# Optimization experiments

Hardware: AMD Instinct MI355X
Metric: run time of the kernel (lower is better)

## Reference

```python
import jax, jax.numpy as jnp
import numpy as np

T, B, I, H = 512, 64, 1024, 1024


def setup_inputs() -> dict:
    key = jax.random.key(0)
    k1, k2, k3, k4, k5, k6 = jax.random.split(key, 6)
    bound = 1.0 / np.sqrt(H)  # torch RNNCell init: U(-1/sqrt(H), 1/sqrt(H))
    return {
        "input": jax.random.normal(k1, (T, B, I), dtype=jnp.float32),
        "hidden": jax.random.normal(k2, (B, H), dtype=jnp.float32),
        "W_ih": jax.random.uniform(k3, (H, I), minval=-bound, maxval=bound, dtype=jnp.float32),
        "W_hh": jax.random.uniform(k4, (H, H), minval=-bound, maxval=bound, dtype=jnp.float32),
        "b_ih": jax.random.uniform(k5, (H,), minval=-bound, maxval=bound, dtype=jnp.float32),
        "b_hh": jax.random.uniform(k6, (H,), minval=-bound, maxval=bound, dtype=jnp.float32),
    }


def reference(input, hidden, W_ih, W_hh, b_ih, b_hh):
    # Precompute input projections for all timesteps in one big GEMM:
    # [T,B,I] @ [I,H] -> [T,B,H]
    x_proj = jnp.einsum("tbi,hi->tbh", input, W_ih) + b_ih + b_hh

    def step(h, xp):
        # h' = tanh(x W_ih^T + b_ih + h W_hh^T + b_hh)
        h_new = jnp.tanh(xp + h @ W_hh.T)
        return h_new, h_new

    h_last, output = jax.lax.scan(step, hidden, x_proj)
    return output, h_last
```

## Files before the change

### kernel.cpp

```cpp
#include <hip/hip_runtime.h>
#include <hip/hip_bf16.h>
#include <math.h>

#define T_STEPS 512
#define BATCH   64
#define IN_DIM  1024
#define HID     1024
#define BH_SZ   (BATCH * HID)

typedef short bf16x8 __attribute__((ext_vector_type(8)));
typedef float f32x4  __attribute__((ext_vector_type(4)));
typedef unsigned u32x4 __attribute__((ext_vector_type(4)));
typedef unsigned long long u64;

__device__ __forceinline__ unsigned ld_coh_u32(const unsigned* p) {
    return __hip_atomic_load(p, __ATOMIC_RELAXED, __HIP_MEMORY_SCOPE_AGENT);
}
__device__ __forceinline__ void st_coh_u32(unsigned* p, unsigned v) {
    __hip_atomic_store(p, v, __ATOMIC_RELAXED, __HIP_MEMORY_SCOPE_AGENT);
}
__device__ __forceinline__ u64 ld_coh_u64(const u64* p) {
    return __hip_atomic_load(p, __ATOMIC_RELAXED, __HIP_MEMORY_SCOPE_AGENT);
}

__device__ __forceinline__ unsigned short f2bf(float x) {
    unsigned u = __builtin_bit_cast(unsigned, x);
    unsigned r = u + 0x7FFFu + ((u >> 16) & 1u);
    return (unsigned short)(r >> 16);
}
__device__ __forceinline__ float bf2f(unsigned short h) {
    unsigned u = ((unsigned)h) << 16;
    return __builtin_bit_cast(float, u);
}
__device__ __forceinline__ float fast_tanh(float x) {
    float e = __expf(2.0f * x);
    return 1.0f - 2.0f * __builtin_amdgcn_rcpf(e + 1.0f);
}

__global__ __launch_bounds__(256) void pack_x_kernel(
    const float* __restrict__ src, unsigned short* __restrict__ dst, int n8)
{
    int idx = blockIdx.x * 256 + threadIdx.x;
    int stride = gridDim.x * 256;
    for (int i = idx; i < n8; i += stride) {
        float4 a = *(const float4*)(src + (size_t)i * 8);
        float4 b = *(const float4*)(src + (size_t)i * 8 + 4);
        float vv[8] = {a.x, a.y, a.z, a.w, b.x, b.y, b.z, b.w};
        bf16x8 o;
        #pragma unroll
        for (int e = 0; e < 8; e++) o[e] = (short)f2bf(vv[e]);
        *(bf16x8*)(dst + (size_t)i * 8) = o;
    }
}

__global__ __launch_bounds__(512, 1) void rnn_fused_kernel(
    const float* __restrict__ x,
    const unsigned short* __restrict__ xp16,
    const float* __restrict__ h0,
    const float* __restrict__ W_ih,
    const float* __restrict__ Whh,
    const float* __restrict__ b_ih,
    const float* __restrict__ b_hh,
    float* __restrict__ out,
    unsigned* hcomm,
    unsigned* flags)
{
    __shared__ unsigned short Wih[16 * 1024];
    __shared__ unsigned short Hhi[16 * 1024];
    __shared__ unsigned short Hlo[16 * 1024];
    __shared__ unsigned short Xh [16 * 1024];
    __shared__ f32x4 Pred[8][64];

    const int bid = blockIdx.x;
    const int j0 = (bid & 63) * 16;
    const int b0 = (bid >> 6) * 16;
    const int tid  = threadIdx.x;
    const int lane = tid & 63;
    const int w    = tid >> 6;

    const int frow = lane & 15;
    const int ksub = (lane >> 4) * 8;
    const int sw   = (frow & 7) << 3;

    #pragma unroll
    for (int i = 0; i < 4; i++) {
        int c = i * 512 + tid;
        int row = c >> 7;
        int k0 = (c & 127) * 8;
        const float* src = W_ih + (size_t)(j0 + row) * IN_DIM + k0;
        float4 v0 = *(const float4*)(src);
        float4 v1 = *(const float4*)(src + 4);
        float vv[8] = {v0.x, v0.y, v0.z, v0.w, v1.x, v1.y, v1.z, v1.w};
        bf16x8 hi8;
        #pragma unroll
        for (int e = 0; e < 8; e++) hi8[e] = (short)f2bf(vv[e]);
        int ofs = row * 1024 + (k0 ^ ((row & 7) << 3));
        *(bf16x8*)&Wih[ofs] = hi8;
    }

    #pragma unroll
    for (int i = 0; i < 4; i++) {
        int c = i * 512 + tid;
        int row = c >> 7;
        int k0 = (c & 127) * 8;
        const float* src = Whh + (size_t)(j0 + row) * HID + k0;
        float4 v0 = *(const float4*)(src);
        float4 v1 = *(const float4*)(src + 4);
        float vv[8] = {v0.x, v0.y, v0.z, v0.w, v1.x, v1.y, v1.z, v1.w};
        bf16x8 hi8, lo8;
        #pragma unroll
        for (int e = 0; e < 8; e++) {
            unsigned short h = f2bf(vv[e]);
            hi8[e] = (short)h;
            lo8[e] = (short)f2bf(vv[e] - bf2f(h));
        }
        int ofs = row * 1024 + (k0 ^ ((row & 7) << 3));
        *(bf16x8*)&Hhi[ofs] = hi8;
        *(bf16x8*)&Hlo[ofs] = lo8;
    }
    __syncthreads();
    bf16x8 wh[4], wl[4];
    #pragma unroll
    for (int kk = 0; kk < 4; kk++) {
        int kidx = w * 128 + kk * 32 + ksub;
        int ofs  = frow * 1024 + (kidx ^ sw);
        wh[kk] = *(const bf16x8*)&Hhi[ofs];
        wl[kk] = *(const bf16x8*)&Hlo[ofs];
    }
    __syncthreads();

    if (xp16) {
        #pragma unroll
        for (int i = 0; i < 4; i++) {
            int c = i * 512 + tid;
            int row = c >> 7;
            int k0 = (c & 127) * 8;
            bf16x8 hi8 = *(const bf16x8*)(xp16 + (size_t)(b0 + row) * IN_DIM + k0);
            int ofs = row * 1024 + (k0 ^ ((row & 7) << 3));
            *(bf16x8*)&Xh[ofs] = hi8;
        }
    } else {
        #pragma unroll
        for (int i = 0; i < 4; i++) {
            int c = i * 512 + tid;
            int row = c >> 7;
            int k0 = (c & 127) * 8;
            const float* p = x + (size_t)(b0 + row) * IN_DIM + k0;
            float4 v0 = *(const float4*)(p);
            float4 v1 = *(const float4*)(p + 4);
            float vv[8] = {v0.x, v0.y, v0.z, v0.w, v1.x, v1.y, v1.z, v1.w};
            bf16x8 hi8;
            #pragma unroll
            for (int e = 0; e < 8; e++) hi8[e] = (short)f2bf(vv[e]);
            int ofs = row * 1024 + (k0 ^ ((row & 7) << 3));
            *(bf16x8*)&Xh[ofs] = hi8;
        }
    }

    const int o = tid;
    const size_t out_off = (size_t)(b0 + (o >> 4)) * HID + (size_t)(j0 + (o & 15));
    float bias = 0.f;
    if (tid < 256) bias = b_ih[j0 + (o & 15)] + b_hh[j0 + (o & 15)];

    for (int t = 0; t < T_STEPS; t++) {
        if (t == 0) {
            #pragma unroll
            for (int i = 0; i < 4; i++) {
                int c = i * 512 + tid;
                int row = c >> 7;
                int k0 = (c & 127) * 8;
                const float* p = h0 + (size_t)(b0 + row) * HID + k0;
                float4 v0 = *(const float4*)(p);
                float4 v1 = *(const float4*)(p + 4);
                float vv[8] = {v0.x, v0.y, v0.z, v0.w, v1.x, v1.y, v1.z, v1.w};
                bf16x8 hi8, lo8;
                #pragma unroll
                for (int e = 0; e < 8; e++) {
                    unsigned short h = f2bf(vv[e]);
                    hi8[e] = (short)h;
                    lo8[e] = (short)f2bf(vv[e] - bf2f(h));
                }
                int ofs = row * 1024 + (k0 ^ ((row & 7) << 3));
                *(bf16x8*)&Hhi[ofs] = hi8;
                *(bf16x8*)&Hlo[ofs] = lo8;
            }
        } else {
            const u64* hsrc64 = (const u64*)(hcomm + (size_t)((t + 1) & 1) * BH_SZ);
            u64 pv[16];
            #pragma unroll
            for (int i = 0; i < 4; i++) {
                int c = i * 512 + tid;
                int row = c >> 7;
                int k0 = (c & 127) * 8;
                const u64* p = hsrc64 + (((size_t)(b0 + row) * HID + k0) >> 1);
                #pragma unroll
                for (int e = 0; e < 4; e++)
                    pv[i * 4 + e] = ld_coh_u64(p + e);
            }
            #pragma unroll
            for (int i = 0; i < 4; i++) {
                int c = i * 512 + tid;
                int row = c >> 7;
                int k0 = (c & 127) * 8;
                u32x4 hiu, lou;
                #pragma unroll
                for (int e = 0; e < 4; e++) {
                    u64 q = pv[i * 4 + e];
                    unsigned p0 = (unsigned)q;
                    unsigned p1 = (unsigned)(q >> 32);
                    hiu[e] = (p0 & 0xFFFFu) | (p1 << 16);
                    lou[e] = (p0 >> 16) | (p1 & 0xFFFF0000u);
                }
                int ofs = row * 1024 + (k0 ^ ((row & 7) << 3));
                *(u32x4*)&Hhi[ofs] = hiu;
                *(u32x4*)&Hlo[ofs] = lou;
            }
        }
        __syncthreads();

        {
            f32x4 acc0 = {0.f, 0.f, 0.f, 0.f};
            f32x4 acc1 = {0.f, 0.f, 0.f, 0.f};
            #pragma unroll
            for (int kk = 0; kk < 4; kk++) {
                int kidx = w * 128 + kk * 32 + ksub;
                int ofs  = frow * 1024 + (kidx ^ sw);
                bf16x8 ahi = *(const bf16x8*)&Hhi[ofs];
                bf16x8 alo = *(const bf16x8*)&Hlo[ofs];
                bf16x8 xh  = *(const bf16x8*)&Xh[ofs];
                bf16x8 wi  = *(const bf16x8*)&Wih[ofs];
                acc0 = __builtin_amdgcn_mfma_f32_16x16x32_bf16(ahi, wh[kk], acc0, 0, 0, 0);
                acc1 = __builtin_amdgcn_mfma_f32_16x16x32_bf16(ahi, wl[kk], acc1, 0, 0, 0);
                acc0 = __builtin_amdgcn_mfma_f32_16x16x32_bf16(alo, wh[kk], acc0, 0, 0, 0);
                acc1 = __builtin_amdgcn_mfma_f32_16x16x32_bf16(xh,  wi,     acc1, 0, 0, 0);
            }
            Pred[w][lane] = acc0 + acc1;
        }
        __syncthreads();

        float hn = 0.f;
        if (tid < 256) {
            const int b = o >> 4, j = o & 15;
            const int plane = ((b >> 2) << 4) | j;
            const int pr = b & 3;
            float s = bias;
            #pragma unroll
            for (int k = 0; k < 8; k++) s += Pred[k][plane][pr];
            hn = fast_tanh(s);
            unsigned short hi = f2bf(hn);
            unsigned short lo = f2bf(hn - bf2f(hi));
            unsigned pk = (unsigned)hi | ((unsigned)lo << 16);
            st_coh_u32(hcomm + (size_t)(t & 1) * BH_SZ + out_off, pk);
        }
        __syncthreads();

        if (tid == 0) st_coh_u32(&flags[bid * 32], (unsigned)(t + 1));

        if (tid < 256) {
            out[(size_t)t * BH_SZ + out_off] = hn;
            if (t == T_STEPS - 1)
                out[(size_t)T_STEPS * BH_SZ + out_off] = hn;
        }
        if (t + 1 < T_STEPS) {
            if (xp16) {
                const unsigned short* xs = xp16 + (size_t)(t + 1) * BH_SZ;
                #pragma unroll
                for (int i = 0; i < 4; i++) {
                    int c = i * 512 + tid;
                    int row = c >> 7;
                    int k0 = (c & 127) * 8;
                    bf16x8 hi8 = *(const bf16x8*)(xs + (size_t)(b0 + row) * IN_DIM + k0);
                    int ofs = row * 1024 + (k0 ^ ((row & 7) << 3));
                    *(bf16x8*)&Xh[ofs] = hi8;
                }
            } else {
                const float* xs = x + (size_t)(t + 1) * BH_SZ;
                #pragma unroll
                for (int i = 0; i < 4; i++) {
                    int c = i * 512 + tid;
                    int row = c >> 7;
                    int k0 = (c & 127) * 8;
                    const float* p = xs + (size_t)(b0 + row) * IN_DIM + k0;
                    float4 v0 = *(const float4*)(p);
                    float4 v1 = *(const float4*)(p + 4);
                    float vv[8] = {v0.x, v0.y, v0.z, v0.w, v1.x, v1.y, v1.z, v1.w};
                    bf16x8 hi8;
                    #pragma unroll
                    for (int e = 0; e < 8; e++) hi8[e] = (short)f2bf(vv[e]);
                    int ofs = row * 1024 + (k0 ^ ((row & 7) << 3));
                    *(bf16x8*)&Xh[ofs] = hi8;
                }
            }
        }

        if (tid < 64) {
            const unsigned target = (unsigned)(t + 1);
            for (;;) {
                int ok = 1;
                #pragma unroll
                for (int g = 0; g < 4; g++) {
                    unsigned v = ld_coh_u32(&flags[(size_t)(tid + g * 64) * 32]);
                    ok &= (v >= target) ? 1 : 0;
                }
                if (__all(ok)) break;
                __builtin_amdgcn_s_sleep(4);
            }
        }
        __syncthreads();
    }
}

extern "C" void kernel_launch(void* const* d_in, const int* in_sizes, int n_in,
                              void* d_out, int out_size, void* d_ws, size_t ws_size,
                              hipStream_t stream)
{
    const float* input  = (const float*)d_in[0];
    const float* hidden = (const float*)d_in[1];
    const float* W_ih   = (const float*)d_in[2];
    const float* W_hh   = (const float*)d_in[3];
    const float* b_ih   = (const float*)d_in[4];
    const float* b_hh   = (const float*)d_in[5];
    float* out = (float*)d_out;

    unsigned* flags = (unsigned*)d_ws;
    unsigned* hcomm = (unsigned*)((char*)d_ws + 256 * 32 * sizeof(unsigned));
    hipMemsetAsync(flags, 0, 256 * 32 * sizeof(unsigned), stream);

    const size_t xpk_off  = (size_t)1 << 20;
    const size_t xpk_size = (size_t)T_STEPS * BH_SZ * sizeof(unsigned short);
    const unsigned short* xp16 = nullptr;
    if (ws_size >= xpk_off + xpk_size) {
        unsigned short* xp = (unsigned short*)((char*)d_ws + xpk_off);
        pack_x_kernel<<<2048, 256, 0, stream>>>(input, xp,
                                                (T_STEPS * BATCH * IN_DIM) / 8);
        xp16 = xp;
    }

    rnn_fused_kernel<<<256, 512, 0, stream>>>(
        input, xp16, hidden, W_ih, W_hh, b_ih, b_hh, out, hcomm, flags);
}
```

Baseline: 2.311 ms.

## Move epilogue into one wavefront and overlap next-step X load with barrier wait

The per-step epilogue (bias, reduction over partial sums, tanh, hi/lo bf16 packing) now runs in a single wavefront. Each lane handles four outputs and writes them with 64-bit coherent stores and a float4 output store. That wave publishes the flag right after an s_waitcnt, without a block-wide __syncthreads. The other waves stage the next timestep's input tile into LDS while the first wave spins on the grid flags, so one barrier per step is removed and the X load overlaps the inter-block wait. In exchange, the tanh work is concentrated in fewer threads and the X staging is spread over 448 threads with a guarded tail.

New measurement: 2.881 ms. 24.7% more time.

```diff
diff --git a/kernel.cpp b/kernel.cpp
--- a/kernel.cpp
+++ b/kernel.cpp
@@ -22,6 +22,9 @@
 __device__ __forceinline__ u64 ld_coh_u64(const u64* p) {
     return __hip_atomic_load(p, __ATOMIC_RELAXED, __HIP_MEMORY_SCOPE_AGENT);
 }
+__device__ __forceinline__ void st_coh_u64(u64* p, u64 v) {
+    __hip_atomic_store(p, v, __ATOMIC_RELAXED, __HIP_MEMORY_SCOPE_AGENT);
+}
 
 __device__ __forceinline__ unsigned short f2bf(float x) {
     unsigned u = __builtin_bit_cast(unsigned, x);
@@ -35,6 +38,11 @@
 __device__ __forceinline__ float fast_tanh(float x) {
     float e = __expf(2.0f * x);
     return 1.0f - 2.0f * __builtin_amdgcn_rcpf(e + 1.0f);
+}
+__device__ __forceinline__ unsigned pack_hl(float v) {
+    unsigned short hi = f2bf(v);
+    unsigned short lo = f2bf(v - bf2f(hi));
+    return (unsigned)hi | ((unsigned)lo << 16);
 }
 
 __global__ __launch_bounds__(256) void pack_x_kernel(
@@ -157,10 +165,17 @@
         }
     }
 
-    const int o = tid;
-    const size_t out_off = (size_t)(b0 + (o >> 4)) * HID + (size_t)(j0 + (o & 15));
-    float bias = 0.f;
-    if (tid < 256) bias = b_ih[j0 + (o & 15)] + b_hh[j0 + (o & 15)];
+    const int bloc  = lane >> 2;
+    const int jb    = (4 * lane) & 15;
+    const int prr   = bloc & 3;
+    const int pbase = (bloc >> 2) << 4;
+    const size_t woff = (size_t)(b0 + bloc) * HID + j0 + jb;
+    float bias4[4];
+    if (tid < 64) {
+        #pragma unroll
+        for (int i = 0; i < 4; i++)
+            bias4[i] = b_ih[j0 + jb + i] + b_hh[j0 + jb + i];
+    }
 
     for (int t = 0; t < T_STEPS; t++) {
         if (t == 0) {
@@ -238,74 +253,76 @@
         }
         __syncthreads();
 
-        float hn = 0.f;
-        if (tid < 256) {
-            const int b = o >> 4, j = o & 15;
-            const int plane = ((b >> 2) << 4) | j;
-            const int pr = b & 3;
-            float s = bias;
-            #pragma unroll
-            for (int k = 0; k < 8; k++) s += Pred[k][plane][pr];
-            hn = fast_tanh(s);
-            unsigned short hi = f2bf(hn);
-            unsigned short lo = f2bf(hn - bf2f(hi));
-            unsigned pk = (unsigned)hi | ((unsigned)lo << 16);
-            st_coh_u32(hcomm + (size_t)(t & 1) * BH_SZ + out_off, pk);
-        }
-        __syncthreads();
-
-        if (tid == 0) st_coh_u32(&flags[bid * 32], (unsigned)(t + 1));
-
-        if (tid < 256) {
-            out[(size_t)t * BH_SZ + out_off] = hn;
+        if (tid < 64) {
+            float hn4[4];
+            #pragma unroll
+            for (int i = 0; i < 4; i++) {
+                float s = bias4[i];
+                const int plane = pbase | (jb + i);
+                #pragma unroll
+                for (int k = 0; k < 8; k++) s += Pred[k][plane][prr];
+                hn4[i] = fast_tanh(s);
+            }
+            u64* dst = (u64*)(hcomm + (size_t)(t & 1) * BH_SZ + woff);
+            u64 w0 = (u64)pack_hl(hn4[0]) | ((u64)pack_hl(hn4[1]) << 32);
+            u64 w1 = (u64)pack_hl(hn4[2]) | ((u64)pack_hl(hn4[3]) << 32);
+            st_coh_u64(dst, w0);
+            st_coh_u64(dst + 1, w1);
+            asm volatile("s_waitcnt vmcnt(0)" ::: "memory");
+            if (lane == 0) st_coh_u32(&flags[bid * 32], (unsigned)(t + 1));
+            float4 o4 = make_float4(hn4[0], hn4[1], hn4[2], hn4[3]);
+            *(float4*)(out + (size_t)t * BH_SZ + woff) = o4;
             if (t == T_STEPS - 1)
-                out[(size_t)T_STEPS * BH_SZ + out_off] = hn;
-        }
-        if (t + 1 < T_STEPS) {
-            if (xp16) {
-                const unsigned short* xs = xp16 + (size_t)(t + 1) * BH_SZ;
-                #pragma unroll
-                for (int i = 0; i < 4; i++) {
-                    int c = i * 512 + tid;
-                    int row = c >> 7;
-                    int k0 = (c & 127) * 8;
-                    bf16x8 hi8 = *(const bf16x8*)(xs + (size_t)(b0 + row) * IN_DIM + k0);
-                    int ofs = row * 1024 + (k0 ^ ((row & 7) << 3));
-                    *(bf16x8*)&Xh[ofs] = hi8;
-                }
-            } else {
-                const float* xs = x + (size_t)(t + 1) * BH_SZ;
-                #pragma unroll
-                for (int i = 0; i < 4; i++) {
-                    int c = i * 512 + tid;
-                    int row = c >> 7;
-                    int k0 = (c & 127) * 8;
-                    const float* p = xs + (size_t)(b0 + row) * IN_DIM + k0;
-                    float4 v0 = *(const float4*)(p);
-                    float4 v1 = *(const float4*)(p + 4);
-                    float vv[8] = {v0.x, v0.y, v0.z, v0.w, v1.x, v1.y, v1.z, v1.w};
-                    bf16x8 hi8;
-                    #pragma unroll
-                    for (int e = 0; e < 8; e++) hi8[e] = (short)f2bf(vv[e]);
-                    int ofs = row * 1024 + (k0 ^ ((row & 7) << 3));
-                    *(bf16x8*)&Xh[ofs] = hi8;
-                }
-            }
-        }
-
-        if (tid < 64) {
+                *(float4*)(out + (size_t)T_STEPS * BH_SZ + woff) = o4;
             const unsigned target = (unsigned)(t + 1);
             for (;;) {
                 int ok = 1;
                 #pragma unroll
                 for (int g = 0; g < 4; g++) {
-                    unsigned v = ld_coh_u32(&flags[(size_t)(tid + g * 64) * 32]);
+                    unsigned v = ld_coh_u32(&flags[(size_t)(lane + g * 64) * 32]);
                     ok &= (v >= target) ? 1 : 0;
                 }
                 if (__all(ok)) break;
                 __builtin_amdgcn_s_sleep(4);
             }
-        }
+        } else if (t + 1 < T_STEPS) {
+            const int tt = tid - 64;
+            if (xp16) {
+                const unsigned short* xs = xp16 + (size_t)(t + 1) * BH_SZ;
+                #pragma unroll
+                for (int i = 0; i < 5; i++) {
+                    int c = i * 448 + tt;
+                    if (c < 2048) {
+                        int row = c >> 7;
+                        int k0 = (c & 127) * 8;
+                        bf16x8 hi8 = *(const bf16x8*)(xs + (size_t)(b0 + row) * IN_DIM + k0);
+                        int ofs = row * 1024 + (k0 ^ ((row & 7) << 3));
+                        *(bf16x8*)&Xh[ofs] = hi8;
+                    }
+                }
+            } else {
+                const float* xs = x + (size_t)(t + 1) * BH_SZ;
+                #pragma unroll
+                for (int i = 0; i < 5; i++) {
+                    int c = i * 448 + tt;
+                    if (c < 2048) {
+                        int row = c >> 7;
+                        int k0 = (c & 127) * 8;
+                        const float* p = xs + (size_t)(b0 + row) * IN_DIM + k0;
+                        float4 v0 = *(const float4*)(p);
+                        float4 v1 = *(const float4*)(p + 4);
+                        float vv[8] = {v0.x, v0.y, v0.z, v0.w,
+                                       v1.x, v1.y, v1.z, v1.w};
+                        bf16x8 hi8;
+                        #pragma unroll
+                        for (int e = 0; e < 8; e++) hi8[e] = (short)f2bf(vv[e]);
+                        int ofs = row * 1024 + (k0 ^ ((row & 7) << 3));
+                        *(bf16x8*)&Xh[ofs] = hi8;
+                    }
+                }
+            }
+        }
+
         __syncthreads();
     }
 }
```
